# Kernel tuning notes

Hardware: AMD Instinct MI355X
Metric: run time of the kernel (lower is better)

The kernel has to match this reference:

```python
import jax, jax.numpy as jnp
import numpy as np

TOP_K = 2  # config.num_active_experts


def setup_inputs() -> dict:
    key = jax.random.key(0)
    k1, k2, k3, k4 = jax.random.split(key, 4)
    B, S, D = 2, 2048, 1024
    E, W = 8, 1024  # 8 experts, each width 1024 -> total_expert_width = 8192
    x = jax.random.normal(k1, (B, S, D), dtype=jnp.float32)
    router_w = jax.random.normal(k2, (E, D), dtype=jnp.float32) * 0.02
    w1 = jax.random.normal(k3, (D, E * W), dtype=jnp.float32) * 0.02
    w2 = jax.random.normal(k4, (E * W, D), dtype=jnp.float32) * 0.02
    return {"x": x, "router_w": router_w, "w1": w1, "w2": w2}


def reference(x, router_w, w1, w2):
    B, S, D = x.shape
    E = router_w.shape[0]
    W = w1.shape[1] // E  # uniform expert width
    T = B * S
    xf = x.reshape(T, D)

    # Router: sigmoid gating, top-k, sum-normalized weights (norm_topk_prob)
    router_logits = jnp.einsum('td,ed->te', xf, router_w)
    router_probs = jax.nn.sigmoid(router_logits.astype(jnp.float32))
    top_w, sel = jax.lax.top_k(router_probs, TOP_K)          # [T,K]
    top_w = top_w / (top_w.sum(axis=-1, keepdims=True) + 1e-20)
    top_w = top_w.astype(x.dtype)

    # Expert MLPs: expert e uses w1[:, off_e:off_e+W], w2[off_e:off_e+W, :].
    # Uniform width -> single batched einsum over experts (same math as the
    # padded-gather / block-sparse SDD/DSD grouped GEMM pipeline).
    W1e = w1.reshape(D, E, W).transpose(1, 0, 2)             # [E,D,W]
    W2e = w2.reshape(E, W, D)                                # [E,W,D]
    h = jnp.einsum('td,edw->etw', xf, W1e)                   # up-proj
    a = jnp.square(jax.nn.relu(h))                           # relu_squared
    y = jnp.einsum('etw,ewd->etd', a, W2e)                   # down-proj

    # Weighted scatter-combine: combine_weights[t,e] = top_w if e selected else 0
    cw = jnp.zeros((T, E), dtype=x.dtype).at[jnp.arange(T)[:, None], sel].set(top_w)
    out = jnp.einsum('etd,te->td', y, cw)
    return out.reshape(B, S, D)
```

## Files before the change

### kernel.cpp

```cpp
#include <hip/hip_runtime.h>
#include <hip/hip_bf16.h>


#define T_TOKENS 4096
#define DD 1024
#define EE 8
#define WW 1024
#define CAP 1536
#define BM 128
#define BN 64
#define BK 64
#define MT (CAP / BM)
#define NT 16

typedef short bf16x8 __attribute__((ext_vector_type(8)));
typedef float f32x4 __attribute__((ext_vector_type(4)));

__device__ __forceinline__ void gload_lds16(const void* g, void* l) {
  __builtin_amdgcn_global_load_lds((__attribute__((address_space(1))) void*)(g),
                                   (__attribute__((address_space(3))) void*)(l),
                                   16, 0, 0);
}

__device__ __forceinline__ float bf2f(unsigned short u) {
  union { unsigned int i; float f; } v; v.i = (unsigned int)u << 16; return v.f;
}

#define TR_BLOCKS 4096
__global__ __launch_bounds__(256) void pre_kernel(
    const float* __restrict__ w1, const float* __restrict__ w2,
    const float* __restrict__ x, const float* __restrict__ rw,
    __hip_bfloat16* __restrict__ w1t, __hip_bfloat16* __restrict__ w2t,
    __hip_bfloat16* __restrict__ xb, int* __restrict__ sel,
    float* __restrict__ wpair)
{
  __shared__ float tile[64][65];
  int b = blockIdx.x;
  if (b < TR_BLOCKS) {
    int bx = b & 15;
    int by = b >> 4;
    const float* src; __hip_bfloat16* dst;
    long src_ld, dst_ld, c0, r0;
    if (by < 128) {
      src = w1; dst = w1t; src_ld = EE * WW; dst_ld = DD;
      c0 = (long)bx * 64;
      r0 = (long)by * 64;
    } else {
      int z = by - 128;
      int e = z >> 4;
      int yy = z & 15;
      src = w2 + (long)e * WW * DD;
      dst = w2t + (long)e * DD * WW;
      src_ld = DD; dst_ld = WW;
      c0 = (long)bx * 64;
      r0 = (long)yy * 64;
    }
    int tx = threadIdx.x & 15, ty = threadIdx.x >> 4;
#pragma unroll
    for (int i = 0; i < 4; i++) {
      int sr = ty + 16 * i;
      f32x4 v = *(const f32x4*)(src + (c0 + sr) * src_ld + r0 + tx * 4);
      tile[sr][tx * 4 + 0] = v[0];
      tile[sr][tx * 4 + 1] = v[1];
      tile[sr][tx * 4 + 2] = v[2];
      tile[sr][tx * 4 + 3] = v[3];
    }
    __syncthreads();
#pragma unroll
    for (int i = 0; i < 4; i++) {
      int dr = ty + 16 * i;
      union { __hip_bfloat16 hb[4]; ushort4 u4; } pk;
#pragma unroll
      for (int j = 0; j < 4; j++)
        pk.hb[j] = __float2bfloat16(tile[tx * 4 + j][dr]);
      *(ushort4*)((unsigned short*)dst + (r0 + dr) * dst_ld + c0 + tx * 4) = pk.u4;
    }
  } else {
    int lane = threadIdx.x & 63;
    int wave = threadIdx.x >> 6;
    int t = (b - TR_BLOCKS) * 4 + wave;
    const float* xrow = x + (size_t)t * DD;
    float acc[EE];
#pragma unroll
    for (int e = 0; e < EE; e++) acc[e] = 0.f;
#pragma unroll
    for (int i = 0; i < DD / 64; i++) {
      int d = lane + i * 64;
      float xv = xrow[d];
      xb[t * DD + d] = __float2bfloat16(xv);
#pragma unroll
      for (int e = 0; e < EE; e++) acc[e] += xv * rw[e * DD + d];
    }
#pragma unroll
    for (int e = 0; e < EE; e++) {
#pragma unroll
      for (int off = 32; off > 0; off >>= 1)
        acc[e] += __shfl_down(acc[e], off, 64);
    }
    if (lane == 0) {
      float p[EE];
#pragma unroll
      for (int e = 0; e < EE; e++) p[e] = 1.f / (1.f + expf(-acc[e]));
      int e0 = 0; float b0 = p[0];
      for (int e = 1; e < EE; e++) if (p[e] > b0) { b0 = p[e]; e0 = e; }
      int e1 = -1; float b1 = -1.f;
      for (int e = 0; e < EE; e++) {
        if (e == e0) continue;
        if (p[e] > b1) { b1 = p[e]; e1 = e; }
      }
      float s = b0 + b1 + 1e-20f;
      sel[t] = e0 | (e1 << 8);
      wpair[2 * t]     = b0 / s;
      wpair[2 * t + 1] = b1 / s;
    }
  }
}

__global__ __launch_bounds__(1024) void build_lists(
    const int* __restrict__ sel, int* __restrict__ counts,
    int* __restrict__ idx, int* __restrict__ tslot)
{
  __shared__ int lcnt[EE];
  int tid = threadIdx.x, lane = tid & 63;
  if (tid < EE) lcnt[tid] = 0;
  __syncthreads();
  unsigned long long lower = (1ull << lane) - 1;
#pragma unroll
  for (int j = 0; j < T_TOKENS / 1024; j++) {
    int t = j * 1024 + tid;
    int s = sel[t];
    int e0 = s & 0xff, e1 = (s >> 8) & 0xff;
    int slot0 = 0, slot1 = 0;
#pragma unroll
    for (int e = 0; e < EE; e++) {
      unsigned long long m0 = __ballot(e0 == e);
      unsigned long long m1 = __ballot(e1 == e);
      int c0 = __popcll(m0), c1 = __popcll(m1);
      int base = 0;
      if (lane == 0 && (c0 + c1) > 0) base = atomicAdd(&lcnt[e], c0 + c1);
      base = __shfl(base, 0, 64);
      if (e0 == e) slot0 = base + __popcll(m0 & lower);
      if (e1 == e) slot1 = base + c0 + __popcll(m1 & lower);
    }
    int p0 = e0 * CAP + slot0, p1 = e1 * CAP + slot1;
    idx[p0] = t; idx[p1] = t;
    tslot[2 * t] = p0; tslot[2 * t + 1] = p1;
  }
  __syncthreads();
  if (tid < EE) counts[tid] = lcnt[tid];
}

__global__ __launch_bounds__(256) void gemm1_kernel(
    const __hip_bfloat16* __restrict__ xb, const __hip_bfloat16* __restrict__ w1t,
    const int* __restrict__ counts, const int* __restrict__ idx,
    __hip_bfloat16* __restrict__ act)
{
  __shared__ short As[BM * BK];
  __shared__ short Bs[BN * BK];
  int bid = blockIdx.x;
  int e = bid & 7;
  int i = bid >> 3;
  int mt = i >> 4, nt = i & 15;
  int n_e = counts[e];
  if (mt * BM >= n_e) return;

  int tid = threadIdx.x;
  int lane = tid & 63;
  int wave = __builtin_amdgcn_readfirstlane(tid >> 6);
  int wm = (wave >> 1) * 64, wn = (wave & 1) * 32;
  int m16 = lane & 15, qd = lane >> 4;

  const __hip_bfloat16* gA[4];
  const __hip_bfloat16* gB[2];
#pragma unroll
  for (int i2 = 0; i2 < 4; i2++) {
    int s = i2 * 256 + tid;
    int r = s >> 3;
    int q = (s & 7) ^ (r & 7);
    int rowA = mt * BM + r;
    int slot = rowA < n_e ? rowA : n_e - 1;
    int tok = idx[e * CAP + slot];
    gA[i2] = xb + (size_t)tok * DD + q * 8;
  }
#pragma unroll
  for (int i2 = 0; i2 < 2; i2++) {
    int s = i2 * 256 + tid;
    int r = s >> 3;
    int q = (s & 7) ^ (r & 7);
    gB[i2] = w1t + ((size_t)e * WW + nt * BN + r) * DD + q * 8;
  }
  short* ldsA[4];
  short* ldsB[2];
#pragma unroll
  for (int i2 = 0; i2 < 4; i2++) ldsA[i2] = As + (i2 * 256 + wave * 64) * 8;
#pragma unroll
  for (int i2 = 0; i2 < 2; i2++) ldsB[i2] = Bs + (i2 * 256 + wave * 64) * 8;

  int aoff[4][2], boff[2][2];
#pragma unroll
  for (int i2 = 0; i2 < 4; i2++) {
    int r = wm + i2 * 16 + m16;
#pragma unroll
    for (int h = 0; h < 2; h++)
      aoff[i2][h] = (r * 8 + ((qd + h * 4) ^ (r & 7))) * 8;
  }
#pragma unroll
  for (int j = 0; j < 2; j++) {
    int r = wn + j * 16 + m16;
#pragma unroll
    for (int h = 0; h < 2; h++)
      boff[j][h] = (r * 8 + ((qd + h * 4) ^ (r & 7))) * 8;
  }

  f32x4 zero = {0.f, 0.f, 0.f, 0.f};
  f32x4 acc[4][2];
#pragma unroll
  for (int mi = 0; mi < 4; mi++)
#pragma unroll
    for (int ni = 0; ni < 2; ni++) acc[mi][ni] = zero;

  for (int k0 = 0; k0 < DD; k0 += BK) {
    gload_lds16(gA[0] + k0, ldsA[0]);
    gload_lds16(gA[1] + k0, ldsA[1]);
    gload_lds16(gA[2] + k0, ldsA[2]);
    gload_lds16(gA[3] + k0, ldsA[3]);
    gload_lds16(gB[0] + k0, ldsB[0]);
    gload_lds16(gB[1] + k0, ldsB[1]);
    __syncthreads();
#pragma unroll
    for (int h = 0; h < 2; h++) {
      bf16x8 af[4], bfr[2];
#pragma unroll
      for (int i2 = 0; i2 < 4; i2++) af[i2] = *(const bf16x8*)(As + aoff[i2][h]);
#pragma unroll
      for (int j = 0; j < 2; j++) bfr[j] = *(const bf16x8*)(Bs + boff[j][h]);
#pragma unroll
      for (int mi = 0; mi < 4; mi++)
#pragma unroll
        for (int ni = 0; ni < 2; ni++)
          acc[mi][ni] = __builtin_amdgcn_mfma_f32_16x16x32_bf16(
              af[mi], bfr[ni], acc[mi][ni], 0, 0, 0);
    }
    __syncthreads();
  }

#pragma unroll
  for (int mi = 0; mi < 4; mi++) {
#pragma unroll
    for (int reg = 0; reg < 4; reg++) {
      int rowt = mt * BM + wm + mi * 16 + qd * 4 + reg;
      if (rowt < n_e) {
#pragma unroll
        for (int ni = 0; ni < 2; ni++) {
          float v = acc[mi][ni][reg];
          v = v > 0.f ? v * v : 0.f;
          int col = nt * BN + wn + ni * 16 + m16;
          act[((size_t)e * CAP + rowt) * WW + col] = __float2bfloat16(v);
        }
      }
    }
  }
}

__global__ __launch_bounds__(256) void gemm2_kernel(
    const __hip_bfloat16* __restrict__ act, const __hip_bfloat16* __restrict__ w2t,
    const int* __restrict__ counts, __hip_bfloat16* __restrict__ y)
{
  __shared__ short As[BM * BK];
  __shared__ short Bs[BN * BK];
  int bid = blockIdx.x;
  int e = bid & 7;
  int i = bid >> 3;
  int mt = i >> 4, nt = i & 15;
  int n_e = counts[e];
  if (mt * BM >= n_e) return;

  int tid = threadIdx.x;
  int lane = tid & 63;
  int wave = __builtin_amdgcn_readfirstlane(tid >> 6);
  int wm = (wave >> 1) * 64, wn = (wave & 1) * 32;
  int m16 = lane & 15, qd = lane >> 4;

  const __hip_bfloat16* gA[4];
  const __hip_bfloat16* gB[2];
#pragma unroll
  for (int i2 = 0; i2 < 4; i2++) {
    int s = i2 * 256 + tid;
    int r = s >> 3;
    int q = (s & 7) ^ (r & 7);
    gA[i2] = act + ((size_t)e * CAP + mt * BM + r) * WW + q * 8;
  }
#pragma unroll
  for (int i2 = 0; i2 < 2; i2++) {
    int s = i2 * 256 + tid;
    int r = s >> 3;
    int q = (s & 7) ^ (r & 7);
    gB[i2] = w2t + ((size_t)e * DD + nt * BN + r) * WW + q * 8;
  }
  short* ldsA[4];
  short* ldsB[2];
#pragma unroll
  for (int i2 = 0; i2 < 4; i2++) ldsA[i2] = As + (i2 * 256 + wave * 64) * 8;
#pragma unroll
  for (int i2 = 0; i2 < 2; i2++) ldsB[i2] = Bs + (i2 * 256 + wave * 64) * 8;

  int aoff[4][2], boff[2][2];
#pragma unroll
  for (int i2 = 0; i2 < 4; i2++) {
    int r = wm + i2 * 16 + m16;
#pragma unroll
    for (int h = 0; h < 2; h++)
      aoff[i2][h] = (r * 8 + ((qd + h * 4) ^ (r & 7))) * 8;
  }
#pragma unroll
  for (int j = 0; j < 2; j++) {
    int r = wn + j * 16 + m16;
#pragma unroll
    for (int h = 0; h < 2; h++)
      boff[j][h] = (r * 8 + ((qd + h * 4) ^ (r & 7))) * 8;
  }

  f32x4 zero = {0.f, 0.f, 0.f, 0.f};
  f32x4 acc[4][2];
#pragma unroll
  for (int mi = 0; mi < 4; mi++)
#pragma unroll
    for (int ni = 0; ni < 2; ni++) acc[mi][ni] = zero;

  for (int k0 = 0; k0 < WW; k0 += BK) {
    gload_lds16(gA[0] + k0, ldsA[0]);
    gload_lds16(gA[1] + k0, ldsA[1]);
    gload_lds16(gA[2] + k0, ldsA[2]);
    gload_lds16(gA[3] + k0, ldsA[3]);
    gload_lds16(gB[0] + k0, ldsB[0]);
    gload_lds16(gB[1] + k0, ldsB[1]);
    __syncthreads();
#pragma unroll
    for (int h = 0; h < 2; h++) {
      bf16x8 af[4], bfr[2];
#pragma unroll
      for (int i2 = 0; i2 < 4; i2++) af[i2] = *(const bf16x8*)(As + aoff[i2][h]);
#pragma unroll
      for (int j = 0; j < 2; j++) bfr[j] = *(const bf16x8*)(Bs + boff[j][h]);
#pragma unroll
      for (int mi = 0; mi < 4; mi++)
#pragma unroll
        for (int ni = 0; ni < 2; ni++)
          acc[mi][ni] = __builtin_amdgcn_mfma_f32_16x16x32_bf16(
              af[mi], bfr[ni], acc[mi][ni], 0, 0, 0);
    }
    __syncthreads();
  }

#pragma unroll
  for (int mi = 0; mi < 4; mi++) {
#pragma unroll
    for (int reg = 0; reg < 4; reg++) {
      int slot = mt * BM + wm + mi * 16 + qd * 4 + reg;
      if (slot < n_e) {
#pragma unroll
        for (int ni = 0; ni < 2; ni++) {
          int col = nt * BN + wn + ni * 16 + m16;
          y[((size_t)e * CAP + slot) * DD + col] = __float2bfloat16(acc[mi][ni][reg]);
        }
      }
    }
  }
}

__global__ __launch_bounds__(256) void combine_kernel(
    const __hip_bfloat16* __restrict__ y, const int* __restrict__ tslot,
    const float* __restrict__ wpair, float* __restrict__ out)
{
  int t = blockIdx.x;
  int c = threadIdx.x * 4;
  int s0 = tslot[2 * t], s1 = tslot[2 * t + 1];
  float w0 = wpair[2 * t], w1 = wpair[2 * t + 1];
  const unsigned short* yu = (const unsigned short*)y;
  ushort4 a = *(const ushort4*)(yu + (size_t)s0 * DD + c);
  ushort4 bq = *(const ushort4*)(yu + (size_t)s1 * DD + c);
  f32x4 o;
  o[0] = w0 * bf2f(a.x) + w1 * bf2f(bq.x);
  o[1] = w0 * bf2f(a.y) + w1 * bf2f(bq.y);
  o[2] = w0 * bf2f(a.z) + w1 * bf2f(bq.z);
  o[3] = w0 * bf2f(a.w) + w1 * bf2f(bq.w);
  *(f32x4*)(out + (size_t)t * DD + c) = o;
}

extern "C" void kernel_launch(void* const* d_in, const int* in_sizes, int n_in,
                              void* d_out, int out_size, void* d_ws, size_t ws_size,
                              hipStream_t stream)
{
  const float* x  = (const float*)d_in[0];
  const float* rw = (const float*)d_in[1];
  const float* w1 = (const float*)d_in[2];
  const float* w2 = (const float*)d_in[3];
  float* out = (float*)d_out;

  char* ws = (char*)d_ws;
  __hip_bfloat16* xb  = (__hip_bfloat16*)ws;  ws += (size_t)T_TOKENS * DD * 2;
  __hip_bfloat16* w1t = (__hip_bfloat16*)ws;  ws += (size_t)EE * WW * DD * 2;
  __hip_bfloat16* w2t = (__hip_bfloat16*)ws;  ws += (size_t)EE * DD * WW * 2;
  __hip_bfloat16* act = (__hip_bfloat16*)ws;  ws += (size_t)EE * CAP * WW * 2;
  __hip_bfloat16* y   = (__hip_bfloat16*)ws;  ws += (size_t)EE * CAP * DD * 2;
  int*   counts = (int*)ws;                   ws += 256;
  int*   idx    = (int*)ws;                   ws += (size_t)EE * CAP * 4;
  int*   sel    = (int*)ws;                   ws += (size_t)T_TOKENS * 4;
  int*   tslot  = (int*)ws;                   ws += (size_t)T_TOKENS * 8;
  float* wpair  = (float*)ws;                 ws += (size_t)T_TOKENS * 8;

  pre_kernel<<<TR_BLOCKS + T_TOKENS / 4, 256, 0, stream>>>(
      w1, w2, x, rw, w1t, w2t, xb, sel, wpair);
  build_lists<<<1, 1024, 0, stream>>>(sel, counts, idx, tslot);
  gemm1_kernel<<<EE * MT * NT, 256, 0, stream>>>(xb, w1t, counts, idx, act);
  gemm2_kernel<<<EE * MT * NT, 256, 0, stream>>>(act, w2t, counts, y);
  combine_kernel<<<T_TOKENS, 256, 0, stream>>>(y, tslot, wpair, out);
}
```

Measured before the change: 192.7 us.

## Fuse routing into prekernel, overlap w2 transpose with gemm1, widen GEMM tiles

Drops the single-block build_lists kernel: the router now assigns slots directly with global atomics on padded per-expert counters, which are zeroed by a memset. The w2 transpose-convert moves out of pre_kernel and runs as extra blocks of the gemm1 launch, so it can overlap the first GEMM. Both GEMMs go from 128x64 to 128x128 tiles with a 4x4 MFMA accumulator per wave and occupancy hint 3. In exchange, slot order within an expert becomes nondeterministic, register pressure rises, and the tile count halves.

```diff
diff --git a/kernel.cpp b/kernel.cpp
--- a/kernel.cpp
+++ b/kernel.cpp
@@ -8,10 +8,13 @@
 #define WW 1024
 #define CAP 1536
 #define BM 128
-#define BN 64
+#define BN 128
 #define BK 64
 #define MT (CAP / BM)
-#define NT 16
+#define NT (WW / BN)
+#define GEMM_BLOCKS (EE * MT * NT)
+#define TR1_BLOCKS 2048
+#define TR2_BLOCKS 2048
 
 typedef short bf16x8 __attribute__((ext_vector_type(8)));
 typedef float f32x4 __attribute__((ext_vector_type(4)));
@@ -26,35 +29,23 @@
   union { unsigned int i; float f; } v; v.i = (unsigned int)u << 16; return v.f;
 }
 
-#define TR_BLOCKS 4096
 __global__ __launch_bounds__(256) void pre_kernel(
-    const float* __restrict__ w1, const float* __restrict__ w2,
-    const float* __restrict__ x, const float* __restrict__ rw,
-    __hip_bfloat16* __restrict__ w1t, __hip_bfloat16* __restrict__ w2t,
-    __hip_bfloat16* __restrict__ xb, int* __restrict__ sel,
-    float* __restrict__ wpair)
+    const float* __restrict__ w1, const float* __restrict__ x,
+    const float* __restrict__ rw,
+    __hip_bfloat16* __restrict__ w1t, __hip_bfloat16* __restrict__ xb,
+    int* __restrict__ counts, int* __restrict__ idx,
+    int* __restrict__ tslot, float* __restrict__ wpair)
 {
   __shared__ float tile[64][65];
   int b = blockIdx.x;
-  if (b < TR_BLOCKS) {
+  if (b < TR1_BLOCKS) {
     int bx = b & 15;
     int by = b >> 4;
-    const float* src; __hip_bfloat16* dst;
-    long src_ld, dst_ld, c0, r0;
-    if (by < 128) {
-      src = w1; dst = w1t; src_ld = EE * WW; dst_ld = DD;
-      c0 = (long)bx * 64;
-      r0 = (long)by * 64;
-    } else {
-      int z = by - 128;
-      int e = z >> 4;
-      int yy = z & 15;
-      src = w2 + (long)e * WW * DD;
-      dst = w2t + (long)e * DD * WW;
-      src_ld = DD; dst_ld = WW;
-      c0 = (long)bx * 64;
-      r0 = (long)yy * 64;
-    }
+    const float* src = w1;
+    __hip_bfloat16* dst = w1t;
+    long src_ld = EE * WW, dst_ld = DD;
+    long c0 = (long)bx * 64;
+    long r0 = (long)by * 64;
     int tx = threadIdx.x & 15, ty = threadIdx.x >> 4;
 #pragma unroll
     for (int i = 0; i < 4; i++) {
@@ -78,7 +69,7 @@
   } else {
     int lane = threadIdx.x & 63;
     int wave = threadIdx.x >> 6;
-    int t = (b - TR_BLOCKS) * 4 + wave;
+    int t = (b - TR1_BLOCKS) * 4 + wave;
     const float* xrow = x + (size_t)t * DD;
     float acc[EE];
 #pragma unroll
@@ -109,69 +100,74 @@
         if (p[e] > b1) { b1 = p[e]; e1 = e; }
       }
       float s = b0 + b1 + 1e-20f;
-      sel[t] = e0 | (e1 << 8);
+      int s0 = atomicAdd(&counts[e0 * 16], 1);
+      int s1 = atomicAdd(&counts[e1 * 16], 1);
+      int p0 = e0 * CAP + s0, p1 = e1 * CAP + s1;
+      idx[p0] = t; idx[p1] = t;
+      tslot[2 * t] = p0; tslot[2 * t + 1] = p1;
       wpair[2 * t]     = b0 / s;
       wpair[2 * t + 1] = b1 / s;
     }
   }
 }
 
-__global__ __launch_bounds__(1024) void build_lists(
-    const int* __restrict__ sel, int* __restrict__ counts,
-    int* __restrict__ idx, int* __restrict__ tslot)
-{
-  __shared__ int lcnt[EE];
-  int tid = threadIdx.x, lane = tid & 63;
-  if (tid < EE) lcnt[tid] = 0;
-  __syncthreads();
-  unsigned long long lower = (1ull << lane) - 1;
-#pragma unroll
-  for (int j = 0; j < T_TOKENS / 1024; j++) {
-    int t = j * 1024 + tid;
-    int s = sel[t];
-    int e0 = s & 0xff, e1 = (s >> 8) & 0xff;
-    int slot0 = 0, slot1 = 0;
-#pragma unroll
-    for (int e = 0; e < EE; e++) {
-      unsigned long long m0 = __ballot(e0 == e);
-      unsigned long long m1 = __ballot(e1 == e);
-      int c0 = __popcll(m0), c1 = __popcll(m1);
-      int base = 0;
-      if (lane == 0 && (c0 + c1) > 0) base = atomicAdd(&lcnt[e], c0 + c1);
-      base = __shfl(base, 0, 64);
-      if (e0 == e) slot0 = base + __popcll(m0 & lower);
-      if (e1 == e) slot1 = base + c0 + __popcll(m1 & lower);
-    }
-    int p0 = e0 * CAP + slot0, p1 = e1 * CAP + slot1;
-    idx[p0] = t; idx[p1] = t;
-    tslot[2 * t] = p0; tslot[2 * t + 1] = p1;
-  }
-  __syncthreads();
-  if (tid < EE) counts[tid] = lcnt[tid];
-}
-
-__global__ __launch_bounds__(256) void gemm1_kernel(
+__global__ __launch_bounds__(256, 3) void gemm1_kernel(
     const __hip_bfloat16* __restrict__ xb, const __hip_bfloat16* __restrict__ w1t,
     const int* __restrict__ counts, const int* __restrict__ idx,
-    __hip_bfloat16* __restrict__ act)
+    __hip_bfloat16* __restrict__ act,
+    const float* __restrict__ w2, __hip_bfloat16* __restrict__ w2t)
 {
-  __shared__ short As[BM * BK];
-  __shared__ short Bs[BN * BK];
+  __shared__ __attribute__((aligned(16))) char smem[32768];
   int bid = blockIdx.x;
+  if (bid >= GEMM_BLOCKS) {
+    float (*tile)[65] = (float (*)[65])smem;
+    int b2 = bid - GEMM_BLOCKS;
+    int bx = b2 & 15;
+    int z = b2 >> 4;
+    int e = z >> 4, yy = z & 15;
+    const float* src = w2 + (long)e * WW * DD;
+    __hip_bfloat16* dst = w2t + (long)e * DD * WW;
+    long src_ld = DD, dst_ld = WW;
+    long c0 = (long)bx * 64;
+    long r0 = (long)yy * 64;
+    int tx = threadIdx.x & 15, ty = threadIdx.x >> 4;
+#pragma unroll
+    for (int i = 0; i < 4; i++) {
+      int sr = ty + 16 * i;
+      f32x4 v = *(const f32x4*)(src + (c0 + sr) * src_ld + r0 + tx * 4);
+      tile[sr][tx * 4 + 0] = v[0];
+      tile[sr][tx * 4 + 1] = v[1];
+      tile[sr][tx * 4 + 2] = v[2];
+      tile[sr][tx * 4 + 3] = v[3];
+    }
+    __syncthreads();
+#pragma unroll
+    for (int i = 0; i < 4; i++) {
+      int dr = ty + 16 * i;
+      union { __hip_bfloat16 hb[4]; ushort4 u4; } pk;
+#pragma unroll
+      for (int j = 0; j < 4; j++)
+        pk.hb[j] = __float2bfloat16(tile[tx * 4 + j][dr]);
+      *(ushort4*)((unsigned short*)dst + (r0 + dr) * dst_ld + c0 + tx * 4) = pk.u4;
+    }
+    return;
+  }
+  short* As = (short*)smem;
+  short* Bs = (short*)(smem + 16384);
   int e = bid & 7;
   int i = bid >> 3;
-  int mt = i >> 4, nt = i & 15;
-  int n_e = counts[e];
+  int mt = i >> 3, nt = i & 7;
+  int n_e = counts[e * 16];
   if (mt * BM >= n_e) return;
 
   int tid = threadIdx.x;
   int lane = tid & 63;
   int wave = __builtin_amdgcn_readfirstlane(tid >> 6);
-  int wm = (wave >> 1) * 64, wn = (wave & 1) * 32;
+  int wm = (wave >> 1) * 64, wn = (wave & 1) * 64;
   int m16 = lane & 15, qd = lane >> 4;
 
   const __hip_bfloat16* gA[4];
-  const __hip_bfloat16* gB[2];
+  const __hip_bfloat16* gB[4];
 #pragma unroll
   for (int i2 = 0; i2 < 4; i2++) {
     int s = i2 * 256 + tid;
@@ -181,63 +177,56 @@
     int slot = rowA < n_e ? rowA : n_e - 1;
     int tok = idx[e * CAP + slot];
     gA[i2] = xb + (size_t)tok * DD + q * 8;
-  }
-#pragma unroll
-  for (int i2 = 0; i2 < 2; i2++) {
-    int s = i2 * 256 + tid;
-    int r = s >> 3;
-    int q = (s & 7) ^ (r & 7);
     gB[i2] = w1t + ((size_t)e * WW + nt * BN + r) * DD + q * 8;
   }
   short* ldsA[4];
-  short* ldsB[2];
-#pragma unroll
-  for (int i2 = 0; i2 < 4; i2++) ldsA[i2] = As + (i2 * 256 + wave * 64) * 8;
-#pragma unroll
-  for (int i2 = 0; i2 < 2; i2++) ldsB[i2] = Bs + (i2 * 256 + wave * 64) * 8;
-
-  int aoff[4][2], boff[2][2];
+  short* ldsB[4];
 #pragma unroll
   for (int i2 = 0; i2 < 4; i2++) {
-    int r = wm + i2 * 16 + m16;
+    ldsA[i2] = As + (i2 * 256 + wave * 64) * 8;
+    ldsB[i2] = Bs + (i2 * 256 + wave * 64) * 8;
+  }
+
+  int aoff[4][2], boff[4][2];
+#pragma unroll
+  for (int mi = 0; mi < 4; mi++) {
+    int r = wm + mi * 16 + m16;
 #pragma unroll
     for (int h = 0; h < 2; h++)
-      aoff[i2][h] = (r * 8 + ((qd + h * 4) ^ (r & 7))) * 8;
-  }
-#pragma unroll
-  for (int j = 0; j < 2; j++) {
-    int r = wn + j * 16 + m16;
+      aoff[mi][h] = (r * 8 + ((qd + h * 4) ^ (r & 7))) * 8;
+  }
+#pragma unroll
+  for (int ni = 0; ni < 4; ni++) {
+    int r = wn + ni * 16 + m16;
 #pragma unroll
     for (int h = 0; h < 2; h++)
-      boff[j][h] = (r * 8 + ((qd + h * 4) ^ (r & 7))) * 8;
+      boff[ni][h] = (r * 8 + ((qd + h * 4) ^ (r & 7))) * 8;
   }
 
   f32x4 zero = {0.f, 0.f, 0.f, 0.f};
-  f32x4 acc[4][2];
+  f32x4 acc[4][4];
 #pragma unroll
   for (int mi = 0; mi < 4; mi++)
 #pragma unroll
-    for (int ni = 0; ni < 2; ni++) acc[mi][ni] = zero;
+    for (int ni = 0; ni < 4; ni++) acc[mi][ni] = zero;
 
   for (int k0 = 0; k0 < DD; k0 += BK) {
-    gload_lds16(gA[0] + k0, ldsA[0]);
-    gload_lds16(gA[1] + k0, ldsA[1]);
-    gload_lds16(gA[2] + k0, ldsA[2]);
-    gload_lds16(gA[3] + k0, ldsA[3]);
-    gload_lds16(gB[0] + k0, ldsB[0]);
-    gload_lds16(gB[1] + k0, ldsB[1]);
+#pragma unroll
+    for (int i2 = 0; i2 < 4; i2++) gload_lds16(gA[i2] + k0, ldsA[i2]);
+#pragma unroll
+    for (int i2 = 0; i2 < 4; i2++) gload_lds16(gB[i2] + k0, ldsB[i2]);
     __syncthreads();
 #pragma unroll
     for (int h = 0; h < 2; h++) {
-      bf16x8 af[4], bfr[2];
-#pragma unroll
-      for (int i2 = 0; i2 < 4; i2++) af[i2] = *(const bf16x8*)(As + aoff[i2][h]);
-#pragma unroll
-      for (int j = 0; j < 2; j++) bfr[j] = *(const bf16x8*)(Bs + boff[j][h]);
+      bf16x8 af[4], bfr[4];
+#pragma unroll
+      for (int mi = 0; mi < 4; mi++) af[mi] = *(const bf16x8*)(As + aoff[mi][h]);
+#pragma unroll
+      for (int ni = 0; ni < 4; ni++) bfr[ni] = *(const bf16x8*)(Bs + boff[ni][h]);
 #pragma unroll
       for (int mi = 0; mi < 4; mi++)
 #pragma unroll
-        for (int ni = 0; ni < 2; ni++)
+        for (int ni = 0; ni < 4; ni++)
           acc[mi][ni] = __builtin_amdgcn_mfma_f32_16x16x32_bf16(
               af[mi], bfr[ni], acc[mi][ni], 0, 0, 0);
     }
@@ -251,7 +240,7 @@
       int rowt = mt * BM + wm + mi * 16 + qd * 4 + reg;
       if (rowt < n_e) {
 #pragma unroll
-        for (int ni = 0; ni < 2; ni++) {
+        for (int ni = 0; ni < 4; ni++) {
           float v = acc[mi][ni][reg];
           v = v > 0.f ? v * v : 0.f;
           int col = nt * BN + wn + ni * 16 + m16;
@@ -262,90 +251,84 @@
   }
 }
 
-__global__ __launch_bounds__(256) void gemm2_kernel(
+__global__ __launch_bounds__(256, 3) void gemm2_kernel(
     const __hip_bfloat16* __restrict__ act, const __hip_bfloat16* __restrict__ w2t,
     const int* __restrict__ counts, __hip_bfloat16* __restrict__ y)
 {
-  __shared__ short As[BM * BK];
-  __shared__ short Bs[BN * BK];
+  __shared__ __attribute__((aligned(16))) char smem[32768];
+  short* As = (short*)smem;
+  short* Bs = (short*)(smem + 16384);
   int bid = blockIdx.x;
   int e = bid & 7;
   int i = bid >> 3;
-  int mt = i >> 4, nt = i & 15;
-  int n_e = counts[e];
+  int mt = i >> 3, nt = i & 7;
+  int n_e = counts[e * 16];
   if (mt * BM >= n_e) return;
 
   int tid = threadIdx.x;
   int lane = tid & 63;
   int wave = __builtin_amdgcn_readfirstlane(tid >> 6);
-  int wm = (wave >> 1) * 64, wn = (wave & 1) * 32;
+  int wm = (wave >> 1) * 64, wn = (wave & 1) * 64;
   int m16 = lane & 15, qd = lane >> 4;
 
   const __hip_bfloat16* gA[4];
-  const __hip_bfloat16* gB[2];
+  const __hip_bfloat16* gB[4];
 #pragma unroll
   for (int i2 = 0; i2 < 4; i2++) {
     int s = i2 * 256 + tid;
     int r = s >> 3;
     int q = (s & 7) ^ (r & 7);
     gA[i2] = act + ((size_t)e * CAP + mt * BM + r) * WW + q * 8;
-  }
-#pragma unroll
-  for (int i2 = 0; i2 < 2; i2++) {
-    int s = i2 * 256 + tid;
-    int r = s >> 3;
-    int q = (s & 7) ^ (r & 7);
     gB[i2] = w2t + ((size_t)e * DD + nt * BN + r) * WW + q * 8;
   }
   short* ldsA[4];
-  short* ldsB[2];
-#pragma unroll
-  for (int i2 = 0; i2 < 4; i2++) ldsA[i2] = As + (i2 * 256 + wave * 64) * 8;
-#pragma unroll
-  for (int i2 = 0; i2 < 2; i2++) ldsB[i2] = Bs + (i2 * 256 + wave * 64) * 8;
-
-  int aoff[4][2], boff[2][2];
+  short* ldsB[4];
 #pragma unroll
   for (int i2 = 0; i2 < 4; i2++) {
-    int r = wm + i2 * 16 + m16;
+    ldsA[i2] = As + (i2 * 256 + wave * 64) * 8;
+    ldsB[i2] = Bs + (i2 * 256 + wave * 64) * 8;
+  }
+
+  int aoff[4][2], boff[4][2];
+#pragma unroll
+  for (int mi = 0; mi < 4; mi++) {
+    int r = wm + mi * 16 + m16;
 #pragma unroll
     for (int h = 0; h < 2; h++)
-      aoff[i2][h] = (r * 8 + ((qd + h * 4) ^ (r & 7))) * 8;
-  }
-#pragma unroll
-  for (int j = 0; j < 2; j++) {
-    int r = wn + j * 16 + m16;
+      aoff[mi][h] = (r * 8 + ((qd + h * 4) ^ (r & 7))) * 8;
+  }
+#pragma unroll
+  for (int ni = 0; ni < 4; ni++) {
+    int r = wn + ni * 16 + m16;
 #pragma unroll
     for (int h = 0; h < 2; h++)
-      boff[j][h] = (r * 8 + ((qd + h * 4) ^ (r & 7))) * 8;
+      boff[ni][h] = (r * 8 + ((qd + h * 4) ^ (r & 7))) * 8;
   }
 
   f32x4 zero = {0.f, 0.f, 0.f, 0.f};
-  f32x4 acc[4][2];
+  f32x4 acc[4][4];
 #pragma unroll
   for (int mi = 0; mi < 4; mi++)
 #pragma unroll
-    for (int ni = 0; ni < 2; ni++) acc[mi][ni] = zero;
+    for (int ni = 0; ni < 4; ni++) acc[mi][ni] = zero;
 
   for (int k0 = 0; k0 < WW; k0 += BK) {
-    gload_lds16(gA[0] + k0, ldsA[0]);
-    gload_lds16(gA[1] + k0, ldsA[1]);
-    gload_lds16(gA[2] + k0, ldsA[2]);
-    gload_lds16(gA[3] + k0, ldsA[3]);
-    gload_lds16(gB[0] + k0, ldsB[0]);
-    gload_lds16(gB[1] + k0, ldsB[1]);
+#pragma unroll
+    for (int i2 = 0; i2 < 4; i2++) gload_lds16(gA[i2] + k0, ldsA[i2]);
+#pragma unroll
+    for (int i2 = 0; i2 < 4; i2++) gload_lds16(gB[i2] + k0, ldsB[i2]);
     __syncthreads();
 #pragma unroll
     for (int h = 0; h < 2; h++) {
-      bf16x8 af[4], bfr[2];
-#pragma unroll
-      for (int i2 = 0; i2 < 4; i2++) af[i2] = *(const bf16x8*)(As + aoff[i2][h]);
-#pragma unroll
-      for (int j = 0; j < 2; j++) bfr[j] = *(const bf16x8*)(Bs + boff[j][h]);
+      bf16x8 af[4], bfr[4];
+#pragma unroll
+      for (int mi = 0; mi < 4; mi++) af[mi] = *(const bf16x8*)(As + aoff[mi][h]);
+#pragma unroll
+      for (int ni = 0; ni < 4; ni++) bfr[ni] = *(const bf16x8*)(Bs + boff[ni][h]);
 #pragma unroll
       for (int mi = 0; mi < 4; mi++)
 #pragma unroll
-        for (int ni = 0; ni < 2; ni++)
+        for (int ni = 0; ni < 4; ni++)
           acc[mi][ni] = __builtin_amdgcn_mfma_f32_16x16x32_bf16(
               af[mi], bfr[ni], acc[mi][ni], 0, 0, 0);
     }
@@ -359,7 +342,7 @@
       int slot = mt * BM + wm + mi * 16 + qd * 4 + reg;
       if (slot < n_e) {
 #pragma unroll
-        for (int ni = 0; ni < 2; ni++) {
+        for (int ni = 0; ni < 4; ni++) {
           int col = nt * BN + wn + ni * 16 + m16;
           y[((size_t)e * CAP + slot) * DD + col] = __float2bfloat16(acc[mi][ni][reg]);
         }
@@ -403,16 +386,16 @@
   __hip_bfloat16* w2t = (__hip_bfloat16*)ws;  ws += (size_t)EE * DD * WW * 2;
   __hip_bfloat16* act = (__hip_bfloat16*)ws;  ws += (size_t)EE * CAP * WW * 2;
   __hip_bfloat16* y   = (__hip_bfloat16*)ws;  ws += (size_t)EE * CAP * DD * 2;
-  int*   counts = (int*)ws;                   ws += 256;
+  int*   counts = (int*)ws;                   ws += 16 * EE * sizeof(int);
   int*   idx    = (int*)ws;                   ws += (size_t)EE * CAP * 4;
-  int*   sel    = (int*)ws;                   ws += (size_t)T_TOKENS * 4;
   int*   tslot  = (int*)ws;                   ws += (size_t)T_TOKENS * 8;
   float* wpair  = (float*)ws;                 ws += (size_t)T_TOKENS * 8;
 
-  pre_kernel<<<TR_BLOCKS + T_TOKENS / 4, 256, 0, stream>>>(
-      w1, w2, x, rw, w1t, w2t, xb, sel, wpair);
-  build_lists<<<1, 1024, 0, stream>>>(sel, counts, idx, tslot);
-  gemm1_kernel<<<EE * MT * NT, 256, 0, stream>>>(xb, w1t, counts, idx, act);
-  gemm2_kernel<<<EE * MT * NT, 256, 0, stream>>>(act, w2t, counts, y);
+  hipMemsetAsync(counts, 0, 16 * EE * sizeof(int), stream);
+  pre_kernel<<<TR1_BLOCKS + T_TOKENS / 4, 256, 0, stream>>>(
+      w1, x, rw, w1t, xb, counts, idx, tslot, wpair);
+  gemm1_kernel<<<GEMM_BLOCKS + TR2_BLOCKS, 256, 0, stream>>>(
+      xb, w1t, counts, idx, act, w2, w2t);
+  gemm2_kernel<<<GEMM_BLOCKS, 256, 0, stream>>>(act, w2t, counts, y);
   combine_kernel<<<T_TOKENS, 256, 0, stream>>>(y, tslot, wpair, out);
 }
```

Result: slower. 197.3 us (+2.4%).
